# Optimization experiments

Hardware: AMD Instinct MI355X
Metric: run time of the kernel (lower is better)

Reference implementation:

```python
import jax, jax.numpy as jnp
import numpy as np


def _safe_div(x, y):
    # avoid NaNs in branches that are masked out by jnp.where
    return x / jnp.where(jnp.abs(y) < 1e-12, 1.0, y)


def _closest_point_region(p, a, b, c):
    """Ericson closest-point-on-triangle, vectorized.
    p: [B,n,1,3]; a,b,c: [B,1,m,3] -> (dist2 [B,n,m], region [B,n,m] int32).
    Region codes: 0=vertA 1=vertB 2=vertC 3=edgeAB 4=edgeAC 5=edgeBC 6=face.
    """
    ab = b - a; ac = c - a; cb = c - b
    ap = p - a; bp = p - b; cp = p - c
    d1 = (ab * ap).sum(-1); d2 = (ac * ap).sum(-1)
    d3 = (ab * bp).sum(-1); d4 = (ac * bp).sum(-1)
    d5 = (ab * cp).sum(-1); d6 = (ac * cp).sum(-1)
    vc = d1 * d4 - d3 * d2
    vb = d5 * d2 - d1 * d6
    va = d3 * d6 - d5 * d4

    # candidate closest points per region
    v_ab = jnp.clip(_safe_div(d1, d1 - d3), 0.0, 1.0)
    v_ac = jnp.clip(_safe_div(d2, d2 - d6), 0.0, 1.0)
    v_bc = jnp.clip(_safe_div(d4 - d3, (d4 - d3) + (d5 - d6)), 0.0, 1.0)
    denom = va + vb + vc
    v_f = _safe_div(vb, denom); w_f = _safe_div(vc, denom)

    q_face = a + v_f[..., None] * ab + w_f[..., None] * ac
    q_ab = a + v_ab[..., None] * ab
    q_ac = a + v_ac[..., None] * ac
    q_bc = b + v_bc[..., None] * cb

    # region conditions (Ericson priority: a, b, ab, c, ac, bc, face)
    cond_a = (d1 <= 0) & (d2 <= 0)
    cond_b = (d3 >= 0) & (d4 <= d3)
    cond_ab = (vc <= 0) & (d1 >= 0) & (d3 <= 0)
    cond_c = (d6 >= 0) & (d5 <= d6)
    cond_ac = (vb <= 0) & (d2 >= 0) & (d6 <= 0)
    cond_bc = (va <= 0) & (d4 - d3 >= 0) & (d5 - d6 >= 0)

    def sel(cond, qc, code, q, region):
        q = jnp.where(cond[..., None], qc, q)
        region = jnp.where(cond, code, region)
        return q, region

    # apply lowest priority first so higher-priority regions overwrite
    q = q_face
    region = jnp.full(q.shape[:-1], 6, dtype=jnp.int32)
    q, region = sel(cond_bc, q_bc, 5, q, region)
    q, region = sel(cond_ac, q_ac, 4, q, region)
    q, region = sel(cond_c, c, 2, q, region)
    q, region = sel(cond_ab, q_ab, 3, q, region)
    q, region = sel(cond_b, b, 1, q, region)
    q, region = sel(cond_a, a, 0, q, region)

    diff = p - q
    dist2 = (diff * diff).sum(-1)  # squared distance, as in chamfer-style kernels
    return dist2, region


def setup_inputs() -> dict:
    key = jax.random.key(0)
    k1, k2, k3, k4 = jax.random.split(key, 4)
    B, n, m = 4, 4096, 512
    xyz1 = jax.random.normal(k1, (B, n, 3), dtype=jnp.float32)
    tri1 = jax.random.normal(k2, (B, m, 3), dtype=jnp.float32)
    tri2 = jax.random.normal(k3, (B, m, 3), dtype=jnp.float32)
    tri3 = jax.random.normal(k4, (B, m, 3), dtype=jnp.float32)
    return {"xyz1": xyz1, "tri1": tri1, "tri2": tri2, "tri3": tri3}


def reference(xyz1, tri1, tri2, tri3):
    p = xyz1[:, :, None, :]       # [B,n,1,3]
    a = tri1[:, None, :, :]       # [B,1,m,3]
    b = tri2[:, None, :, :]
    c = tri3[:, None, :, :]
    dist2, region = _closest_point_region(p, a, b, c)  # [B,n,m]
    index = jnp.argmin(dist2, axis=-1).astype(jnp.int32)            # [B,n]
    dist = jnp.min(dist2, axis=-1)                                  # [B,n]
    point = jnp.take_along_axis(region, index[..., None].astype(jnp.int64), axis=-1)[..., 0]
    return dist, point, index
```

## Files before the change

kernel.cpp:

```cpp
#include <hip/hip_runtime.h>
#include <math.h>

#define BB 4
#define NN 4096
#define MM 512
#define PTS 16
#define NPT 2
#define CHUNKS 32
#define MCHUNK (MM / CHUNKS)
#define TPB 512

__device__ __forceinline__ float safercp(float y) {
    float yy = (fabsf(y) < 1e-12f) ? 1.0f : y;
    return __builtin_amdgcn_rcpf(yy);
}

__device__ __forceinline__ float clip01(float x) {
    return fminf(fmaxf(x, 0.0f), 1.0f);
}

__global__ __launch_bounds__(TPB) void tridist_kernel(
    const float* __restrict__ xyz1, const float* __restrict__ tri1,
    const float* __restrict__ tri2, const float* __restrict__ tri3,
    float* __restrict__ out)
{
    __shared__ float4 sT[MM * 7 + MM / 16];

    const int t  = threadIdx.x;
    const int b  = blockIdx.x >> 7;
    const int pb = blockIdx.x & 127;
    const int pt = t & (PTS - 1);
    const int ch = t >> 4;

    {
        const int jj = t;
        const float* g1 = tri1 + ((size_t)b * MM + jj) * 3;
        const float* g2 = tri2 + ((size_t)b * MM + jj) * 3;
        const float* g3 = tri3 + ((size_t)b * MM + jj) * 3;
        const float ax = g1[0], ay = g1[1], az = g1[2];
        const float bx = g2[0], by = g2[1], bz = g2[2];
        const float cx = g3[0], cy = g3[1], cz = g3[2];
        const float abx = bx-ax, aby = by-ay, abz = bz-az;
        const float acx = cx-ax, acy = cy-ay, acz = cz-az;
        const float cbx = cx-bx, cby = cy-by, cbz = cz-bz;
        const float aba  = fmaf(abz, az, fmaf(aby, ay, abx*ax));
        const float abb  = fmaf(abz, bz, fmaf(aby, by, abx*bx));
        const float abc_ = fmaf(abz, cz, fmaf(aby, cy, abx*cx));
        const float aca  = fmaf(acz, az, fmaf(acy, ay, acx*ax));
        const float acb_ = fmaf(acz, bz, fmaf(acy, by, acx*bx));
        const float acc_ = fmaf(acz, cz, fmaf(acy, cy, acx*cx));
        const float ab2  = fmaf(abz, abz, fmaf(aby, aby, abx*abx));
        const float ac2  = fmaf(acz, acz, fmaf(acy, acy, acx*acx));
        const float cb2  = fmaf(cbz, cbz, fmaf(cby, cby, cbx*cbx));
        const float abac = fmaf(abz, acz, fmaf(aby, acy, abx*acx));
        const float gdet = fmaf(ab2, ac2, -(abac*abac));
        const int base = jj * 7 + (jj >> 4);
        sT[base + 0] = make_float4(ax, ay, az, bx);
        sT[base + 1] = make_float4(by, bz, cx, cy);
        sT[base + 2] = make_float4(cz, abx, aby, abz);
        sT[base + 3] = make_float4(acx, acy, acz, cbx);
        sT[base + 4] = make_float4(cby, cbz, aba, abb);
        sT[base + 5] = make_float4(abc_, aca, acb_, acc_);
        sT[base + 6] = make_float4(safercp(ab2), safercp(ac2), safercp(cb2), safercp(gdet));
    }
    __syncthreads();

    float px[NPT], py[NPT], pz[NPT];
#pragma unroll
    for (int np = 0; np < NPT; ++np) {
        const int gi = b * NN + pb * 32 + np * PTS + pt;
        px[np] = xyz1[gi*3 + 0];
        py[np] = xyz1[gi*3 + 1];
        pz[np] = xyz1[gi*3 + 2];
    }

    float bestd[NPT] = {INFINITY, INFINITY};
    int   bestc[NPT] = {0, 0};

    for (int i = 0; i < MCHUNK; ++i) {
        const int j = ch * MCHUNK + i;
        const int base = j * 7 + ch;
        const float4 r0 = sT[base + 0];
        const float4 r1 = sT[base + 1];
        const float4 r2 = sT[base + 2];
        const float4 r3 = sT[base + 3];
        const float4 r4 = sT[base + 4];
        const float4 r5 = sT[base + 5];
        const float4 r6 = sT[base + 6];
        const float ax = r0.x, ay = r0.y, az = r0.z;
        const float bx = r0.w, by = r1.x, bz = r1.y;
        const float cx = r1.z, cy = r1.w, cz = r2.x;
        const float abx = r2.y, aby = r2.z, abz = r2.w;
        const float acx = r3.x, acy = r3.y, acz = r3.z;
        const float cbx = r3.w, cby = r4.x, cbz = r4.y;
        const float aba = r4.z, abb = r4.w;
        const float abc_ = r5.x, aca = r5.y, acb_ = r5.z, acc_ = r5.w;
        const float rab2 = r6.x, rac2 = r6.y, rcb2 = r6.z, rden = r6.w;

#pragma unroll
        for (int np = 0; np < NPT; ++np) {
            const float s1 = fmaf(abz, pz[np], fmaf(aby, py[np], abx*px[np]));
            const float s2 = fmaf(acz, pz[np], fmaf(acy, py[np], acx*px[np]));
            const float d1 = s1 - aba, d3 = s1 - abb, d5 = s1 - abc_;
            const float d2 = s2 - aca, d4 = s2 - acb_, d6 = s2 - acc_;

            const float vc = fmaf(d1, d4, -(d3*d2));
            const float vb = fmaf(d5, d2, -(d1*d6));
            const float va = fmaf(d3, d6, -(d5*d4));

            const float t43 = d4 - d3;
            const float t56 = d5 - d6;

            const float v_ab = clip01(d1 * rab2);
            const float v_ac = clip01(d2 * rac2);
            const float v_bc = clip01(t43 * rcb2);
            const float v_f = vb * rden;
            const float w_f = vc * rden;

            float qx = fmaf(w_f, acx, fmaf(v_f, abx, ax));
            float qy = fmaf(w_f, acy, fmaf(v_f, aby, ay));
            float qz = fmaf(w_f, acz, fmaf(v_f, abz, az));
            int reg = 6;

            const bool c_bc = (va <= 0.0f) && (t43 >= 0.0f) && (t56 >= 0.0f);
            if (c_bc) { qx = fmaf(v_bc, cbx, bx); qy = fmaf(v_bc, cby, by); qz = fmaf(v_bc, cbz, bz); reg = 5; }
            const bool c_ac = (vb <= 0.0f) && (d2 >= 0.0f) && (d6 <= 0.0f);
            if (c_ac) { qx = fmaf(v_ac, acx, ax); qy = fmaf(v_ac, acy, ay); qz = fmaf(v_ac, acz, az); reg = 4; }
            const bool c_c = (d6 >= 0.0f) && (d5 <= d6);
            if (c_c) { qx = cx; qy = cy; qz = cz; reg = 2; }
            const bool c_ab = (vc <= 0.0f) && (d1 >= 0.0f) && (d3 <= 0.0f);
            if (c_ab) { qx = fmaf(v_ab, abx, ax); qy = fmaf(v_ab, aby, ay); qz = fmaf(v_ab, abz, az); reg = 3; }
            const bool c_b = (d3 >= 0.0f) && (d4 <= d3);
            if (c_b) { qx = bx; qy = by; qz = bz; reg = 1; }
            const bool c_a = (d1 <= 0.0f) && (d2 <= 0.0f);
            if (c_a) { qx = ax; qy = ay; qz = az; reg = 0; }

            const float dx = px[np] - qx;
            const float dy = py[np] - qy;
            const float dz = pz[np] - qz;
            const float dist2 = fmaf(dz, dz, fmaf(dy, dy, dx*dx));

            if (dist2 < bestd[np]) { bestd[np] = dist2; bestc[np] = (j << 3) | reg; }
        }
    }

    __syncthreads();
    float* rdu = (float*)sT;
    int*   rcu = (int*)(rdu + NPT * TPB);
#pragma unroll
    for (int np = 0; np < NPT; ++np) {
        rdu[np * TPB + t] = bestd[np];
        rcu[np * TPB + t] = bestc[np];
    }
    __syncthreads();

    if (t < 32) {
        const int np = t >> 4;
        const int p  = t & 15;
        float bd = INFINITY; int bc = 0;
        for (int k = 0; k < CHUNKS; ++k) {
            const float dk = rdu[np * TPB + k * PTS + p];
            const int   ck = rcu[np * TPB + k * PTS + p];
            if (dk < bd) { bd = dk; bc = ck; }
        }
        const int gidx = b * NN + pb * 32 + t;
        out[gidx]             = bd;
        out[BB*NN + gidx]     = (float)(bc & 7);
        out[2*BB*NN + gidx]   = (float)(bc >> 3);
    }
}

extern "C" void kernel_launch(void* const* d_in, const int* in_sizes, int n_in,
                              void* d_out, int out_size, void* d_ws, size_t ws_size,
                              hipStream_t stream) {
    const float* xyz1 = (const float*)d_in[0];
    const float* tri1 = (const float*)d_in[1];
    const float* tri2 = (const float*)d_in[2];
    const float* tri3 = (const float*)d_in[3];
    float* out = (float*)d_out;

    dim3 grid(BB * (NN / 32));
    dim3 block(TPB);
    tridist_kernel<<<grid, block, 0, stream>>>(xyz1, tri1, tri2, tri3, out);
}
```

Measured before the change: 79.69 us.

## Replace region branching with min over edge distances and recompute winner exactly

The inner loop no longer runs the priority cascade of region selects. For each triangle it computes the squared distance to the three clamped edge projections and to the face projection, then picks the face distance when the barycentric signs say the point is inside and the minimum edge distance otherwise. Only the winning triangle index is tracked. The region code and exact distance are recomputed once per point with a reference-matching, non-contracted routine. The per-chunk reduction now uses wavefront shuffles before a smaller shared-memory pass, and the triangle layout in shared memory is reordered so the hot loop reads six float4 instead of seven. The aim is fewer instructions and less divergence in the hot loop. The risk is that near-ties may pick a different argmin than the reference.

```diff
diff --git a/kernel.cpp b/kernel.cpp
--- a/kernel.cpp
+++ b/kernel.cpp
@@ -15,8 +15,70 @@
     return __builtin_amdgcn_rcpf(yy);
 }
 
+__device__ __forceinline__ float safediv(float x, float y) {
+    float yy = (fabsf(y) < 1e-12f) ? 1.0f : y;
+    return x / yy;
+}
+
 __device__ __forceinline__ float clip01(float x) {
     return fminf(fmaxf(x, 0.0f), 1.0f);
+}
+
+__device__ void exact_pair(float px, float py, float pz,
+                           float ax, float ay, float az,
+                           float bx, float by, float bz,
+                           float cx, float cy, float cz,
+                           float* dist2_out, int* reg_out) {
+#pragma clang fp contract(off)
+    const float abx = bx-ax, aby = by-ay, abz = bz-az;
+    const float acx = cx-ax, acy = cy-ay, acz = cz-az;
+    const float cbx = cx-bx, cby = cy-by, cbz = cz-bz;
+    const float apx = px-ax, apy = py-ay, apz = pz-az;
+    const float bpx = px-bx, bpy = py-by, bpz = pz-bz;
+    const float cpx = px-cx, cpy = py-cy, cpz = pz-cz;
+
+    const float d1 = abx*apx + aby*apy + abz*apz;
+    const float d2 = acx*apx + acy*apy + acz*apz;
+    const float d3 = abx*bpx + aby*bpy + abz*bpz;
+    const float d4 = acx*bpx + acy*bpy + acz*bpz;
+    const float d5 = abx*cpx + aby*cpy + abz*cpz;
+    const float d6 = acx*cpx + acy*cpy + acz*cpz;
+
+    const float vc = d1*d4 - d3*d2;
+    const float vb = d5*d2 - d1*d6;
+    const float va = d3*d6 - d5*d4;
+
+    const float v_ab = clip01(safediv(d1, d1 - d3));
+    const float v_ac = clip01(safediv(d2, d2 - d6));
+    const float t43 = d4 - d3;
+    const float t56 = d5 - d6;
+    const float v_bc = clip01(safediv(t43, t43 + t56));
+    const float denom = va + vb + vc;
+    const float v_f = safediv(vb, denom);
+    const float w_f = safediv(vc, denom);
+
+    float qx = ax + v_f*abx + w_f*acx;
+    float qy = ay + v_f*aby + w_f*acy;
+    float qz = az + v_f*abz + w_f*acz;
+    int reg = 6;
+    const bool c_bc = (va <= 0.0f) && (t43 >= 0.0f) && (t56 >= 0.0f);
+    if (c_bc) { qx = bx + v_bc*cbx; qy = by + v_bc*cby; qz = bz + v_bc*cbz; reg = 5; }
+    const bool c_ac = (vb <= 0.0f) && (d2 >= 0.0f) && (d6 <= 0.0f);
+    if (c_ac) { qx = ax + v_ac*acx; qy = ay + v_ac*acy; qz = az + v_ac*acz; reg = 4; }
+    const bool c_c = (d6 >= 0.0f) && (d5 <= d6);
+    if (c_c) { qx = cx; qy = cy; qz = cz; reg = 2; }
+    const bool c_ab = (vc <= 0.0f) && (d1 >= 0.0f) && (d3 <= 0.0f);
+    if (c_ab) { qx = ax + v_ab*abx; qy = ay + v_ab*aby; qz = az + v_ab*abz; reg = 3; }
+    const bool c_b = (d3 >= 0.0f) && (d4 <= d3);
+    if (c_b) { qx = bx; qy = by; qz = bz; reg = 1; }
+    const bool c_a = (d1 <= 0.0f) && (d2 <= 0.0f);
+    if (c_a) { qx = ax; qy = ay; qz = az; reg = 0; }
+
+    const float dx = px - qx;
+    const float dy = py - qy;
+    const float dz = pz - qz;
+    *dist2_out = dx*dx + dy*dy + dz*dz;
+    *reg_out = reg;
 }
 
 __global__ __launch_bounds__(TPB) void tridist_kernel(
@@ -25,6 +87,8 @@
     float* __restrict__ out)
 {
     __shared__ float4 sT[MM * 7 + MM / 16];
+    __shared__ float  sPd[NPT][128];
+    __shared__ int    sPj[NPT][128];
 
     const int t  = threadIdx.x;
     const int b  = blockIdx.x >> 7;
@@ -55,13 +119,13 @@
         const float abac = fmaf(abz, acz, fmaf(aby, acy, abx*acx));
         const float gdet = fmaf(ab2, ac2, -(abac*abac));
         const int base = jj * 7 + (jj >> 4);
-        sT[base + 0] = make_float4(ax, ay, az, bx);
-        sT[base + 1] = make_float4(by, bz, cx, cy);
-        sT[base + 2] = make_float4(cz, abx, aby, abz);
-        sT[base + 3] = make_float4(acx, acy, acz, cbx);
-        sT[base + 4] = make_float4(cby, cbz, aba, abb);
-        sT[base + 5] = make_float4(abc_, aca, acb_, acc_);
-        sT[base + 6] = make_float4(safercp(ab2), safercp(ac2), safercp(cb2), safercp(gdet));
+        sT[base + 0] = make_float4(ax, ay, az, safercp(gdet));
+        sT[base + 1] = make_float4(abx, aby, abz, safercp(ab2));
+        sT[base + 2] = make_float4(acx, acy, acz, safercp(ac2));
+        sT[base + 3] = make_float4(cbx, cby, cbz, safercp(cb2));
+        sT[base + 4] = make_float4(aba, abb, abc_, cx);
+        sT[base + 5] = make_float4(aca, acb_, acc_, cy);
+        sT[base + 6] = make_float4(bx, by, bz, cz);
     }
     __syncthreads();
 
@@ -75,7 +139,7 @@
     }
 
     float bestd[NPT] = {INFINITY, INFINITY};
-    int   bestc[NPT] = {0, 0};
+    int   bestj[NPT] = {0, 0};
 
     for (int i = 0; i < MCHUNK; ++i) {
         const int j = ch * MCHUNK + i;
@@ -86,16 +150,12 @@
         const float4 r3 = sT[base + 3];
         const float4 r4 = sT[base + 4];
         const float4 r5 = sT[base + 5];
-        const float4 r6 = sT[base + 6];
-        const float ax = r0.x, ay = r0.y, az = r0.z;
-        const float bx = r0.w, by = r1.x, bz = r1.y;
-        const float cx = r1.z, cy = r1.w, cz = r2.x;
-        const float abx = r2.y, aby = r2.z, abz = r2.w;
-        const float acx = r3.x, acy = r3.y, acz = r3.z;
-        const float cbx = r3.w, cby = r4.x, cbz = r4.y;
-        const float aba = r4.z, abb = r4.w;
-        const float abc_ = r5.x, aca = r5.y, acb_ = r5.z, acc_ = r5.w;
-        const float rab2 = r6.x, rac2 = r6.y, rcb2 = r6.z, rden = r6.w;
+        const float ax = r0.x, ay = r0.y, az = r0.z, rden = r0.w;
+        const float abx = r1.x, aby = r1.y, abz = r1.z, rab2 = r1.w;
+        const float acx = r2.x, acy = r2.y, acz = r2.z, rac2 = r2.w;
+        const float cbx = r3.x, cby = r3.y, cbz = r3.z, rcb2 = r3.w;
+        const float aba = r4.x, abb = r4.y, abc_ = r4.z;
+        const float aca = r5.x, acb_ = r5.y, acc_ = r5.z;
 
 #pragma unroll
         for (int np = 0; np < NPT; ++np) {
@@ -107,9 +167,7 @@
             const float vc = fmaf(d1, d4, -(d3*d2));
             const float vb = fmaf(d5, d2, -(d1*d6));
             const float va = fmaf(d3, d6, -(d5*d4));
-
             const float t43 = d4 - d3;
-            const float t56 = d5 - d6;
 
             const float v_ab = clip01(d1 * rab2);
             const float v_ac = clip01(d2 * rac2);
@@ -117,56 +175,73 @@
             const float v_f = vb * rden;
             const float w_f = vc * rden;
 
-            float qx = fmaf(w_f, acx, fmaf(v_f, abx, ax));
-            float qy = fmaf(w_f, acy, fmaf(v_f, aby, ay));
-            float qz = fmaf(w_f, acz, fmaf(v_f, abz, az));
-            int reg = 6;
-
-            const bool c_bc = (va <= 0.0f) && (t43 >= 0.0f) && (t56 >= 0.0f);
-            if (c_bc) { qx = fmaf(v_bc, cbx, bx); qy = fmaf(v_bc, cby, by); qz = fmaf(v_bc, cbz, bz); reg = 5; }
-            const bool c_ac = (vb <= 0.0f) && (d2 >= 0.0f) && (d6 <= 0.0f);
-            if (c_ac) { qx = fmaf(v_ac, acx, ax); qy = fmaf(v_ac, acy, ay); qz = fmaf(v_ac, acz, az); reg = 4; }
-            const bool c_c = (d6 >= 0.0f) && (d5 <= d6);
-            if (c_c) { qx = cx; qy = cy; qz = cz; reg = 2; }
-            const bool c_ab = (vc <= 0.0f) && (d1 >= 0.0f) && (d3 <= 0.0f);
-            if (c_ab) { qx = fmaf(v_ab, abx, ax); qy = fmaf(v_ab, aby, ay); qz = fmaf(v_ab, abz, az); reg = 3; }
-            const bool c_b = (d3 >= 0.0f) && (d4 <= d3);
-            if (c_b) { qx = bx; qy = by; qz = bz; reg = 1; }
-            const bool c_a = (d1 <= 0.0f) && (d2 <= 0.0f);
-            if (c_a) { qx = ax; qy = ay; qz = az; reg = 0; }
-
-            const float dx = px[np] - qx;
-            const float dy = py[np] - qy;
-            const float dz = pz[np] - qz;
-            const float dist2 = fmaf(dz, dz, fmaf(dy, dy, dx*dx));
-
-            if (dist2 < bestd[np]) { bestd[np] = dist2; bestc[np] = (j << 3) | reg; }
-        }
-    }
-
-    __syncthreads();
-    float* rdu = (float*)sT;
-    int*   rcu = (int*)(rdu + NPT * TPB);
+            const float apx = px[np] - ax, apy = py[np] - ay, apz = pz[np] - az;
+            const float bpx = apx - abx, bpy = apy - aby, bpz = apz - abz;
+
+            float ex = fmaf(-v_ab, abx, apx), ey = fmaf(-v_ab, aby, apy), ez = fmaf(-v_ab, abz, apz);
+            const float dAB = fmaf(ez, ez, fmaf(ey, ey, ex*ex));
+            ex = fmaf(-v_ac, acx, apx); ey = fmaf(-v_ac, acy, apy); ez = fmaf(-v_ac, acz, apz);
+            const float dAC = fmaf(ez, ez, fmaf(ey, ey, ex*ex));
+            ex = fmaf(-v_bc, cbx, bpx); ey = fmaf(-v_bc, cby, bpy); ez = fmaf(-v_bc, cbz, bpz);
+            const float dBC = fmaf(ez, ez, fmaf(ey, ey, ex*ex));
+            ex = fmaf(-w_f, acx, fmaf(-v_f, abx, apx));
+            ey = fmaf(-w_f, acy, fmaf(-v_f, aby, apy));
+            ez = fmaf(-w_f, acz, fmaf(-v_f, abz, apz));
+            const float dF = fmaf(ez, ez, fmaf(ey, ey, ex*ex));
+
+            const bool inside = (va >= 0.0f) && (vb >= 0.0f) && (vc >= 0.0f);
+            const float dseg = fminf(fminf(dAB, dAC), dBC);
+            const float dist2 = inside ? dF : dseg;
+
+            if (dist2 < bestd[np]) { bestd[np] = dist2; bestj[np] = j; }
+        }
+    }
+
 #pragma unroll
     for (int np = 0; np < NPT; ++np) {
-        rdu[np * TPB + t] = bestd[np];
-        rcu[np * TPB + t] = bestc[np];
+        for (int off = 16; off <= 32; off <<= 1) {
+            const float od = __shfl_xor(bestd[np], off, 64);
+            const int   oj = __shfl_xor(bestj[np], off, 64);
+            if (od < bestd[np] || (od == bestd[np] && oj < bestj[np])) {
+                bestd[np] = od; bestj[np] = oj;
+            }
+        }
+    }
+    const int lane = t & 63;
+    const int w    = t >> 6;
+    if (lane < PTS) {
+#pragma unroll
+        for (int np = 0; np < NPT; ++np) {
+            sPd[np][w * PTS + lane] = bestd[np];
+            sPj[np][w * PTS + lane] = bestj[np];
+        }
     }
     __syncthreads();
 
     if (t < 32) {
         const int np = t >> 4;
         const int p  = t & 15;
-        float bd = INFINITY; int bc = 0;
-        for (int k = 0; k < CHUNKS; ++k) {
-            const float dk = rdu[np * TPB + k * PTS + p];
-            const int   ck = rcu[np * TPB + k * PTS + p];
-            if (dk < bd) { bd = dk; bc = ck; }
-        }
+        float bd = INFINITY; int bj = 0;
+        for (int k = 0; k < 8; ++k) {
+            const float dk = sPd[np][k * PTS + p];
+            const int   jk = sPj[np][k * PTS + p];
+            if (dk < bd || (dk == bd && jk < bj)) { bd = dk; bj = jk; }
+        }
+        const int base = bj * 7 + (bj >> 4);
+        const float4 r0 = sT[base + 0];
+        const float4 r4 = sT[base + 4];
+        const float4 r5 = sT[base + 5];
+        const float4 r6 = sT[base + 6];
         const int gidx = b * NN + pb * 32 + t;
-        out[gidx]             = bd;
-        out[BB*NN + gidx]     = (float)(bc & 7);
-        out[2*BB*NN + gidx]   = (float)(bc >> 3);
+        float dist2; int reg;
+        exact_pair(xyz1[gidx*3+0], xyz1[gidx*3+1], xyz1[gidx*3+2],
+                   r0.x, r0.y, r0.z,
+                   r6.x, r6.y, r6.z,
+                   r4.w, r5.w, r6.w,
+                   &dist2, &reg);
+        out[gidx]             = dist2;
+        out[BB*NN + gidx]     = (float)reg;
+        out[2*BB*NN + gidx]   = (float)bj;
     }
 }
 
```

New measurement: 74.25 us. 6.8% less time.
